# Kernel optimization log

Hardware: AMD Instinct MI355X
Metric: run time of the kernel (lower is better)

## Reference

```python
import jax, jax.numpy as jnp
import numpy as np

# --- grid constants (from init_kwargs) ---
VOXEL = jnp.array([0.2, 0.2, 6.0], dtype=jnp.float32)
PC_MIN = jnp.array([-51.2, -51.2, -3.0], dtype=jnp.float32)
PC_MAX = jnp.array([51.2, 51.2, 3.0], dtype=jnp.float32)
NY, NX = 512, 512          # pseudo_image_dims
NSEG = NY * NX             # dense pillar grid used as segment space
BN_EPS = 1e-3


def setup_inputs() -> dict:
    key = jax.random.key(0)
    k1, k2 = jax.random.split(key)
    B, N, C = 2, 100000, 64
    # points roughly spanning the range, slightly beyond so some get filtered
    pts = jax.random.uniform(k1, (B, N, 3), dtype=jnp.float32)
    lo = jnp.array([-56.0, -56.0, -3.5], dtype=jnp.float32)
    hi = jnp.array([56.0, 56.0, 3.5], dtype=jnp.float32)
    points = lo + pts * (hi - lo)
    W = jax.random.normal(k2, (9, C), dtype=jnp.float32) * 0.1
    return {
        "points": points,
        "W": W,
        "gamma": jnp.ones((C,), jnp.float32),
        "beta": jnp.zeros((C,), jnp.float32),
        "running_mean": jnp.zeros((C,), jnp.float32),
        "running_var": jnp.ones((C,), jnp.float32),
    }


def _embed_one(pts, W, gamma, beta, r_mean, r_var):
    # pts: [N,3] -> pseudo-image [C, NY, NX]
    coords = jnp.floor((pts - PC_MIN) / VOXEL).astype(jnp.int32)        # [N,3] (x,y,z)
    in_range = jnp.all((pts >= PC_MIN) & (pts < PC_MAX), axis=-1)       # [N]
    pid = coords[:, 1] * NX + coords[:, 0]                              # pillar id = y*nx + x
    pid = jnp.where(in_range, pid, 0)
    w = in_range.astype(pts.dtype)[:, None]                             # [N,1] mask weight

    cnt = jax.ops.segment_sum(w[:, 0], pid, num_segments=NSEG)          # [NSEG]
    safe_cnt = jnp.maximum(cnt, 1.0)

    # cluster center offset: per-pillar mean of xyz
    sum_xyz = jax.ops.segment_sum(pts * w, pid, num_segments=NSEG)      # [NSEG,3]
    mean_xyz = sum_xyz / safe_cnt[:, None]
    f_cluster = pts - mean_xyz[pid]

    # voxel center offset
    center = (coords.astype(pts.dtype) + 0.5) * VOXEL + PC_MIN
    f_center = pts - center

    feats = jnp.concatenate([pts, f_cluster, f_center], axis=-1)        # [N,9]

    # PFN layer: Linear(9->C, no bias) + BN1d (eval, running stats) + ReLU
    h = feats @ W                                                       # [N,C]
    h = (h - r_mean) * jax.lax.rsqrt(r_var + BN_EPS) * gamma + beta
    h = jax.nn.relu(h)

    # scatter-avg per pillar, then dense canvas
    vsum = jax.ops.segment_sum(h * w, pid, num_segments=NSEG)           # [NSEG,C]
    vfeat = vsum / safe_cnt[:, None]
    return vfeat.reshape(NY, NX, -1).transpose(2, 0, 1)                 # [C,NY,NX]


def reference(points, W, gamma, beta, running_mean, running_var):
    # points: [B,N,3] -> pseudo-image [B,C,NY,NX]
    return jax.vmap(_embed_one, in_axes=(0, None, None, None, None, None))(
        points, W, gamma, beta, running_mean, running_var)
```

## Files before the change

### kernel.cpp

```cpp
#include <hip/hip_runtime.h>
#include <math.h>

#define NXg 512
#define NYg 512
#define NSEG (NXg * NYg)
#define CCH 64
#define CAP 16
#define ECAP 15
#define SLOTS 4
#define PSTR 5
#define PPB 64
#define BN_EPS 1e-3f

#define PCMINX (-51.2f)
#define PCMINY (-51.2f)
#define PCMINZ (-3.0f)
#define PCMAXX (51.2f)
#define PCMAXY (51.2f)
#define PCMAXZ (3.0f)
#define VOXX (0.2f)
#define VOXY (0.2f)
#define VOXZ (6.0f)

#define RECIPX 5.0f
#define RECIPY 5.0f
#define RECIPZ (__uint_as_float(0x3E2AAAABu))

typedef float nt_float4 __attribute__((ext_vector_type(4)));

__device__ __forceinline__ int calc_pid(float x, float y, float z) {
    bool in_range = (x >= PCMINX) && (x < PCMAXX) &&
                    (y >= PCMINY) && (y < PCMAXY) &&
                    (z >= PCMINZ) && (z < PCMAXZ);
    if (!in_range) return -1;
    int cx = (int)floorf((x - PCMINX) * RECIPX);
    int cy = (int)floorf((y - PCMINY) * RECIPY);
    int p = cy * NXg + cx;
    return (p >= 0 && p < NSEG) ? p : -1;
}

__global__ void k1_bin(const float* __restrict__ pts, unsigned* __restrict__ cnt,
                       float4* __restrict__ first, float4* __restrict__ ext,
                       int B, int N) {
    int i = blockIdx.x * blockDim.x + threadIdx.x;
    if (i >= B * N) return;
    const float* p = pts + (size_t)i * 3;
    float x = p[0], y = p[1], z = p[2];
    int pd = calc_pid(x, y, z);
    if (pd < 0) return;
    int b = i / N;
    int g = b * NSEG + pd;
    unsigned slot = atomicAdd(&cnt[g], 1u);
    float4 e; e.x = x; e.y = y; e.z = z; e.w = 0.0f;
    if (slot == 0) first[g] = e;
    else if (slot < CAP) ext[(size_t)g * ECAP + (slot - 1)] = e;
}

__global__ void __launch_bounds__(256) k4_compute(
    const unsigned* __restrict__ cnt, const float4* __restrict__ first,
    const float4* __restrict__ ext,
    const float* __restrict__ W, const float* __restrict__ gamma,
    const float* __restrict__ beta, const float* __restrict__ rmean,
    const float* __restrict__ rvar, float* __restrict__ out) {
    __shared__ float pxs[PPB * PSTR];
    __shared__ float pys[PPB * PSTR];
    __shared__ float pzs[PPB * PSTR];
    __shared__ float mxs[PPB], mys[PPB], mzs[PPB];
    __shared__ int ks[PPB];
    __shared__ float tileb[CCH * 65];

    int t = threadIdx.x;
    int lane = t & 63;
    int wave = t >> 6;
    int gp0 = (int)blockIdx.x * PPB;

    float w0 = W[0 * CCH + lane], w1 = W[1 * CCH + lane], w2 = W[2 * CCH + lane];
    float w3 = W[3 * CCH + lane], w4 = W[4 * CCH + lane], w5 = W[5 * CCH + lane];
    float w6 = W[6 * CCH + lane], w7 = W[7 * CCH + lane], w8 = W[8 * CCH + lane];
    float sc = gamma[lane] * (1.0f / sqrtf(rvar[lane] + BN_EPS));
    float shift = beta[lane] - rmean[lane] * sc;
    float Ac = (w0 + w3 + w6) * sc;
    float Bc = (w1 + w4 + w7) * sc;
    float Cc = (w2 + w5) * sc;
    float s3 = w3 * sc, s4 = w4 * sc, s5 = w5 * sc;
    float s6 = w6 * sc, s7 = w7 * sc, s8 = w8 * sc;

    if (t < PPB) {
        int gp = gp0 + t;
        float4 f0 = first[gp];
        unsigned kc = cnt[gp];
        int k = (kc < CAP) ? (int)kc : CAP;
        ks[t] = k;
        float sx = 0.f, sy = 0.f, sz = 0.f;
        if (k > 0) {
            sx = f0.x; sy = f0.y; sz = f0.z;
            pxs[t * PSTR + 0] = f0.x;
            pys[t * PSTR + 0] = f0.y;
            pzs[t * PSTR + 0] = f0.z;
            const float4* ex = ext + (size_t)gp * ECAP;
            for (int j = 1; j < k; ++j) {
                float4 e = ex[j - 1];
                if (j < SLOTS) {
                    pxs[t * PSTR + j] = e.x;
                    pys[t * PSTR + j] = e.y;
                    pzs[t * PSTR + j] = e.z;
                }
                sx += e.x; sy += e.y; sz += e.z;
            }
        }
        float fk = (k > 0) ? (float)k : 1.0f;
        mxs[t] = sx / fk; mys[t] = sy / fk; mzs[t] = sz / fk;
    }
    __syncthreads();

    for (int it = 0; it < 16; ++it) {
        int ppl = wave * 16 + it;
        int k = ks[ppl];
        float acc = 0.0f;
        if (k > 0) {
            float mx = mxs[ppl], my = mys[ppl], mz = mzs[ppl];
            int pid = (gp0 + ppl) & (NSEG - 1);
            float ctx = ((float)(pid & (NXg - 1)) + 0.5f) * VOXX + PCMINX;
            float cty = ((float)(pid >> 9) + 0.5f) * VOXY + PCMINY;
            float D = shift;
            D = fmaf(-mx, s3, D); D = fmaf(-my, s4, D); D = fmaf(-mz, s5, D);
            D = fmaf(-ctx, s6, D); D = fmaf(-cty, s7, D);
            int kl = (k < SLOTS) ? k : SLOTS;
            for (int j = 0; j < kl; ++j) {
                float x = pxs[ppl * PSTR + j];
                float y = pys[ppl * PSTR + j];
                float z = pzs[ppl * PSTR + j];
                float cz = floorf((z - PCMINZ) * RECIPZ);
                float ctz = (cz + 0.5f) * VOXZ + PCMINZ;
                float h = fmaf(x, Ac, fmaf(y, Bc, fmaf(z, Cc, fmaf(z - ctz, s8, D))));
                acc += fmaxf(h, 0.0f);
            }
            for (int j = SLOTS; j < k; ++j) {
                float4 e = ext[(size_t)(gp0 + ppl) * ECAP + (j - 1)];
                float cz = floorf((e.z - PCMINZ) * RECIPZ);
                float ctz = (cz + 0.5f) * VOXZ + PCMINZ;
                float h = fmaf(e.x, Ac, fmaf(e.y, Bc, fmaf(e.z, Cc,
                              fmaf(e.z - ctz, s8, D))));
                acc += fmaxf(h, 0.0f);
            }
            acc /= (float)k;
        }
        tileb[lane * 65 + ppl] = acc;
    }
    __syncthreads();

    int b = gp0 >> 18;
    int pbatch = gp0 & (NSEG - 1);
    size_t obase = (size_t)b * CCH * NSEG + (size_t)pbatch;
    for (int jj = 0; jj < 4; ++jj) {
        int idx = jj * 256 + t;
        int c = idx >> 4;
        int q = idx & 15;
        nt_float4 v;
        v.x = tileb[c * 65 + q * 4 + 0];
        v.y = tileb[c * 65 + q * 4 + 1];
        v.z = tileb[c * 65 + q * 4 + 2];
        v.w = tileb[c * 65 + q * 4 + 3];
        __builtin_nontemporal_store(
            v, reinterpret_cast<nt_float4*>(out + obase + (size_t)c * NSEG + q * 4));
    }
}

extern "C" void kernel_launch(void* const* d_in, const int* in_sizes, int n_in,
                              void* d_out, int out_size, void* d_ws, size_t ws_size,
                              hipStream_t stream) {
    const float* points = (const float*)d_in[0];
    const float* W      = (const float*)d_in[1];
    const float* gamma  = (const float*)d_in[2];
    const float* beta   = (const float*)d_in[3];
    const float* rmean  = (const float*)d_in[4];
    const float* rvar   = (const float*)d_in[5];
    float* out = (float*)d_out;

    int B = out_size / (CCH * NSEG);
    int N = in_sizes[0] / (3 * B);
    int BN = B * NSEG;
    int total_pts = B * N;

    unsigned* cnt = (unsigned*)d_ws;
    float4* first = (float4*)(cnt + BN);
    float4* ext   = first + BN;

    (void)hipMemsetAsync(cnt, 0, (size_t)BN * sizeof(unsigned), stream);

    int blk = 256;
    int grd_pts = (total_pts + blk - 1) / blk;
    k1_bin<<<grd_pts, blk, 0, stream>>>(points, cnt, first, ext, B, N);
    k4_compute<<<BN / PPB, blk, 0, stream>>>(cnt, first, ext, W, gamma, beta,
                                             rmean, rvar, out);
}
```

Measured before the change: 46.96 us.

## Parallelize pillar gather across four lanes and precompute z-center offsets in binning

The binning kernel now computes each point's z-offset from its voxel center and stores it in the spare fourth component of the point record. The compute kernel moves to 1024-thread blocks covering 256 pillars. Four lanes now gather each pillar's first points and reduce their sums with shuffles, replacing one thread looping serially. Fewer points are cached in LDS, and the transpose tile grows to match the larger block. The aim is to cut the serial gather latency and repeated floor math, at the cost of much larger LDS use per block and possibly lower occupancy.

```diff
diff --git a/kernel.cpp b/kernel.cpp
--- a/kernel.cpp
+++ b/kernel.cpp
@@ -7,9 +7,10 @@
 #define CCH 64
 #define CAP 16
 #define ECAP 15
-#define SLOTS 4
-#define PSTR 5
-#define PPB 64
+#define LSLOT 2
+#define PPB 256
+#define BLK 1024
+#define TSTR 257
 #define BN_EPS 1e-3f
 
 #define PCMINX (-51.2f)
@@ -51,23 +52,26 @@
     int b = i / N;
     int g = b * NSEG + pd;
     unsigned slot = atomicAdd(&cnt[g], 1u);
-    float4 e; e.x = x; e.y = y; e.z = z; e.w = 0.0f;
+    float cz = floorf((z - PCMINZ) * RECIPZ);
+    float ctz = (cz + 0.5f) * VOXZ + PCMINZ;
+    float4 e; e.x = x; e.y = y; e.z = z; e.w = z - ctz;
     if (slot == 0) first[g] = e;
     else if (slot < CAP) ext[(size_t)g * ECAP + (slot - 1)] = e;
 }
 
-__global__ void __launch_bounds__(256) k4_compute(
+__global__ void __launch_bounds__(BLK, 8) k4_compute(
     const unsigned* __restrict__ cnt, const float4* __restrict__ first,
     const float4* __restrict__ ext,
     const float* __restrict__ W, const float* __restrict__ gamma,
     const float* __restrict__ beta, const float* __restrict__ rmean,
     const float* __restrict__ rvar, float* __restrict__ out) {
-    __shared__ float pxs[PPB * PSTR];
-    __shared__ float pys[PPB * PSTR];
-    __shared__ float pzs[PPB * PSTR];
+    __shared__ float pxs[LSLOT][PPB];
+    __shared__ float pys[LSLOT][PPB];
+    __shared__ float pzs[LSLOT][PPB];
+    __shared__ float pws[LSLOT][PPB];
     __shared__ float mxs[PPB], mys[PPB], mzs[PPB];
     __shared__ int ks[PPB];
-    __shared__ float tileb[CCH * 65];
+    __shared__ float tileb[CCH * TSTR];
 
     int t = threadIdx.x;
     int lane = t & 63;
@@ -85,31 +89,33 @@
     float s3 = w3 * sc, s4 = w4 * sc, s5 = w5 * sc;
     float s6 = w6 * sc, s7 = w7 * sc, s8 = w8 * sc;
 
-    if (t < PPB) {
-        int gp = gp0 + t;
-        float4 f0 = first[gp];
+    {
+        int p = t >> 2;
+        int s = t & 3;
+        int gp = gp0 + p;
         unsigned kc = cnt[gp];
         int k = (kc < CAP) ? (int)kc : CAP;
-        ks[t] = k;
-        float sx = 0.f, sy = 0.f, sz = 0.f;
-        if (k > 0) {
-            sx = f0.x; sy = f0.y; sz = f0.z;
-            pxs[t * PSTR + 0] = f0.x;
-            pys[t * PSTR + 0] = f0.y;
-            pzs[t * PSTR + 0] = f0.z;
-            const float4* ex = ext + (size_t)gp * ECAP;
-            for (int j = 1; j < k; ++j) {
-                float4 e = ex[j - 1];
-                if (j < SLOTS) {
-                    pxs[t * PSTR + j] = e.x;
-                    pys[t * PSTR + j] = e.y;
-                    pzs[t * PSTR + j] = e.z;
-                }
-                sx += e.x; sy += e.y; sz += e.z;
+        float4 e;
+        bool valid;
+        if (s == 0) { e = first[gp]; valid = (k > 0); }
+        else { valid = (s < k); if (valid) e = ext[(size_t)gp * ECAP + (s - 1)]; }
+        float px = valid ? e.x : 0.f;
+        float py = valid ? e.y : 0.f;
+        float pz = valid ? e.z : 0.f;
+        if (valid && s < LSLOT) {
+            pxs[s][p] = e.x; pys[s][p] = e.y; pzs[s][p] = e.z; pws[s][p] = e.w;
+        }
+        px += __shfl_xor(px, 1); py += __shfl_xor(py, 1); pz += __shfl_xor(pz, 1);
+        px += __shfl_xor(px, 2); py += __shfl_xor(py, 2); pz += __shfl_xor(pz, 2);
+        if (s == 0) {
+            for (int j = 4; j < k; ++j) {
+                float4 et = ext[(size_t)gp * ECAP + (j - 1)];
+                px += et.x; py += et.y; pz += et.z;
             }
+            ks[p] = k;
+            float fk = (k > 0) ? (float)k : 1.0f;
+            mxs[p] = px / fk; mys[p] = py / fk; mzs[p] = pz / fk;
         }
-        float fk = (k > 0) ? (float)k : 1.0f;
-        mxs[t] = sx / fk; mys[t] = sy / fk; mzs[t] = sz / fk;
     }
     __syncthreads();
 
@@ -125,27 +131,24 @@
             float D = shift;
             D = fmaf(-mx, s3, D); D = fmaf(-my, s4, D); D = fmaf(-mz, s5, D);
             D = fmaf(-ctx, s6, D); D = fmaf(-cty, s7, D);
-            int kl = (k < SLOTS) ? k : SLOTS;
+            int kl = (k < LSLOT) ? k : LSLOT;
             for (int j = 0; j < kl; ++j) {
-                float x = pxs[ppl * PSTR + j];
-                float y = pys[ppl * PSTR + j];
-                float z = pzs[ppl * PSTR + j];
-                float cz = floorf((z - PCMINZ) * RECIPZ);
-                float ctz = (cz + 0.5f) * VOXZ + PCMINZ;
-                float h = fmaf(x, Ac, fmaf(y, Bc, fmaf(z, Cc, fmaf(z - ctz, s8, D))));
+                float x = pxs[j][ppl];
+                float y = pys[j][ppl];
+                float z = pzs[j][ppl];
+                float zc = pws[j][ppl];
+                float h = fmaf(x, Ac, fmaf(y, Bc, fmaf(z, Cc, fmaf(zc, s8, D))));
                 acc += fmaxf(h, 0.0f);
             }
-            for (int j = SLOTS; j < k; ++j) {
+            for (int j = LSLOT; j < k; ++j) {
                 float4 e = ext[(size_t)(gp0 + ppl) * ECAP + (j - 1)];
-                float cz = floorf((e.z - PCMINZ) * RECIPZ);
-                float ctz = (cz + 0.5f) * VOXZ + PCMINZ;
                 float h = fmaf(e.x, Ac, fmaf(e.y, Bc, fmaf(e.z, Cc,
-                              fmaf(e.z - ctz, s8, D))));
+                              fmaf(e.w, s8, D))));
                 acc += fmaxf(h, 0.0f);
             }
             acc /= (float)k;
         }
-        tileb[lane * 65 + ppl] = acc;
+        tileb[lane * TSTR + ppl] = acc;
     }
     __syncthreads();
 
@@ -153,14 +156,14 @@
     int pbatch = gp0 & (NSEG - 1);
     size_t obase = (size_t)b * CCH * NSEG + (size_t)pbatch;
     for (int jj = 0; jj < 4; ++jj) {
-        int idx = jj * 256 + t;
-        int c = idx >> 4;
-        int q = idx & 15;
+        int idx = jj * BLK + t;
+        int c = idx >> 6;
+        int q = idx & 63;
         nt_float4 v;
-        v.x = tileb[c * 65 + q * 4 + 0];
-        v.y = tileb[c * 65 + q * 4 + 1];
-        v.z = tileb[c * 65 + q * 4 + 2];
-        v.w = tileb[c * 65 + q * 4 + 3];
+        v.x = tileb[c * TSTR + q * 4 + 0];
+        v.y = tileb[c * TSTR + q * 4 + 1];
+        v.z = tileb[c * TSTR + q * 4 + 2];
+        v.w = tileb[c * TSTR + q * 4 + 3];
         __builtin_nontemporal_store(
             v, reinterpret_cast<nt_float4*>(out + obase + (size_t)c * NSEG + q * 4));
     }
@@ -191,6 +194,6 @@
     int blk = 256;
     int grd_pts = (total_pts + blk - 1) / blk;
     k1_bin<<<grd_pts, blk, 0, stream>>>(points, cnt, first, ext, B, N);
-    k4_compute<<<BN / PPB, blk, 0, stream>>>(cnt, first, ext, W, gamma, beta,
+    k4_compute<<<BN / PPB, BLK, 0, stream>>>(cnt, first, ext, W, gamma, beta,
                                              rmean, rvar, out);
 }
```

New measurement: 53.52 us. +14.0%, slower.
